# Performance work log

Hardware: AMD Instinct MI355X
Metric: run time of the kernel (lower is better)

The kernel has to match this reference:

```python
import jax, jax.numpy as jnp
import numpy as np


def setup_inputs() -> dict:
    key = jax.random.key(0)
    k1, k2, k3, k4 = jax.random.split(key, 4)
    B, C, H, W = 4, 512, 64, 64
    K = 20
    Cp = C // 4  # 128, proj_feat output channels
    feat = jax.random.normal(k1, (B, C, H, W), dtype=jnp.float32)
    cam = jax.random.uniform(k2, (B, K, H, W), dtype=jnp.float32)
    # 1x1 conv == linear over channel dim; store kernel as [Cout, Cin]
    w_proj = jax.random.normal(k3, (Cp, C), dtype=jnp.float32) * (1.0 / np.sqrt(C))
    b_proj = jax.random.normal(k4, (Cp,), dtype=jnp.float32) * 0.01
    return {"feat": feat, "cam": cam, "w_proj": w_proj, "b_proj": b_proj}


def reference(feat, cam, w_proj, b_proj):
    B, C, H, W = feat.shape
    K = cam.shape[1]
    N = H * W
    cam_detach = jax.lax.stop_gradient(cam)
    # proj_feat: 1x1 conv -> [B, N, C//4] token layout (matches view+transpose)
    feat_proj = jnp.einsum('bchw,oc->bhwo', feat, w_proj) + b_proj
    feat_proj = feat_proj.reshape(B, N, -1)                      # [B, N, Cp]
    cam_reshape = cam_detach.reshape(B, K, N)                    # [B, K, N]
    class_term = jnp.einsum('bkn,bnd->bkd', cam_reshape, feat_proj)  # [B, K, Cp]
    # unscaled self-attention over N pixels
    pixel_sim = jnp.einsum('bnd,bmd->bnm', feat_proj, feat_proj)     # [B, N, N]
    pixel_sim = jax.nn.softmax(pixel_sim, axis=-1)
    pixel_term = jnp.einsum('bnm,bmd->bnd', pixel_sim, feat_proj)    # [B, N, Cp]
    aug_cam = jnp.einsum('bkd,bnd->bkn', class_term, pixel_term)     # [B, K, N]
    return cam + aug_cam.reshape(B, K, H, W)
```

## Files before the change

### kernel.cpp

```cpp
#include <hip/hip_runtime.h>
#include <hip/hip_bf16.h>
#include <math.h>

#define NB 4
#define NC 512
#define NN 4096
#define NK 20
#define NCP 128
#define SPLIT 4
#define CHUNK (NN / SPLIT)
#define NTILES (CHUNK / 64)

typedef __bf16 bf16x8 __attribute__((ext_vector_type(8)));
typedef float f32x4 __attribute__((ext_vector_type(4)));
typedef float f32x16 __attribute__((ext_vector_type(16)));
typedef short short8 __attribute__((ext_vector_type(8)));
typedef unsigned int uint4v __attribute__((ext_vector_type(4)));

static __device__ __forceinline__ unsigned short f2bf(float f) {
    unsigned int u = __builtin_bit_cast(unsigned int, f);
    unsigned int r = (u + 0x7FFFu + ((u >> 16) & 1u)) >> 16;
    return (unsigned short)r;
}
static __device__ __forceinline__ float bf2f(unsigned short h) {
    unsigned int u = ((unsigned int)h) << 16;
    return __builtin_bit_cast(float, u);
}
static __device__ __forceinline__ bf16x8 ldbf8(const unsigned short* p) {
    return __builtin_bit_cast(bf16x8, *reinterpret_cast<const short8*>(p));
}
static __device__ __forceinline__ void gld16(const unsigned short* g, unsigned short* l) {
    __builtin_amdgcn_global_load_lds(
        (const __attribute__((address_space(1))) unsigned int*)g,
        (__attribute__((address_space(3))) unsigned int*)l, 16, 0, 0);
}
static __device__ __forceinline__ unsigned int cvtpk(float lo, float hi) {
    unsigned int r;
    asm("v_cvt_pk_bf16_f32 %0, %1, %2" : "=v"(r) : "v"(lo), "v"(hi));
    return r;
}

#define MFMA16(a, b, c) __builtin_amdgcn_mfma_f32_16x16x32_bf16(a, b, c, 0, 0, 0)
#define MFMA32(a, b, c) __builtin_amdgcn_mfma_f32_32x32x16_bf16(a, b, c, 0, 0, 0)
#define SCHED0() __builtin_amdgcn_sched_barrier(0)
#define BAR() do { SCHED0(); __builtin_amdgcn_s_barrier(); SCHED0(); } while (0)

__global__ __launch_bounds__(256) void proj_kernel(
    const float* __restrict__ feat, const float* __restrict__ w,
    const float* __restrict__ bias, unsigned short* __restrict__ fp,
    unsigned short* __restrict__ fpT)
{
    const int b = blockIdx.y;
    const int n0 = blockIdx.x * 64;
    const int tid = threadIdx.x;
    const int wid = tid >> 6;
    const int lane = tid & 63;
    const int lg = lane >> 4, lr = lane & 15;

    __shared__ unsigned short lds_f[2][64][40];

    const float* featb = feat + (size_t)b * NC * NN;

    f32x4 acc[2][4];
    #pragma unroll
    for (int i = 0; i < 2; ++i)
        #pragma unroll
        for (int j = 0; j < 4; ++j) acc[i][j] = (f32x4){0.f, 0.f, 0.f, 0.f};

    float4 pre[2];
    #pragma unroll
    for (int it = 0; it < 2; ++it) {
        int idx = it * 256 + tid;
        int cc = idx >> 4, q = idx & 15;
        pre[it] = *reinterpret_cast<const float4*>(&featb[(size_t)cc * NN + n0 + q * 4]);
    }

    for (int c0 = 0; c0 < NC; c0 += 32) {
        const int cur = (c0 >> 5) & 1;
        #pragma unroll
        for (int it = 0; it < 2; ++it) {
            int idx = it * 256 + tid;
            int cc = idx >> 4, q = idx & 15;
            float4 v = pre[it];
            lds_f[cur][q * 4 + 0][cc] = f2bf(v.x);
            lds_f[cur][q * 4 + 1][cc] = f2bf(v.y);
            lds_f[cur][q * 4 + 2][cc] = f2bf(v.z);
            lds_f[cur][q * 4 + 3][cc] = f2bf(v.w);
        }
        __syncthreads();
        if (c0 + 32 < NC) {
            #pragma unroll
            for (int it = 0; it < 2; ++it) {
                int idx = it * 256 + tid;
                int cc = idx >> 4, q = idx & 15;
                pre[it] = *reinterpret_cast<const float4*>(
                    &featb[(size_t)(c0 + 32 + cc) * NN + n0 + q * 4]);
            }
        }
        bf16x8 afr[2];
        #pragma unroll
        for (int dt = 0; dt < 2; ++dt) {
            const float4* wr = reinterpret_cast<const float4*>(
                w + (size_t)(wid * 32 + dt * 16 + lr) * NC + c0 + lg * 8);
            float4 w0 = wr[0], w1 = wr[1];
            short8 a;
            a[0] = (short)f2bf(w0.x); a[1] = (short)f2bf(w0.y);
            a[2] = (short)f2bf(w0.z); a[3] = (short)f2bf(w0.w);
            a[4] = (short)f2bf(w1.x); a[5] = (short)f2bf(w1.y);
            a[6] = (short)f2bf(w1.z); a[7] = (short)f2bf(w1.w);
            afr[dt] = __builtin_bit_cast(bf16x8, a);
        }
        #pragma unroll
        for (int n1 = 0; n1 < 4; ++n1) {
            bf16x8 bfr = ldbf8(&lds_f[cur][n1 * 16 + lr][lg * 8]);
            #pragma unroll
            for (int dt = 0; dt < 2; ++dt)
                acc[dt][n1] = MFMA16(afr[dt], bfr, acc[dt][n1]);
        }
    }
    #pragma unroll
    for (int dt = 0; dt < 2; ++dt)
        #pragma unroll
        for (int n1 = 0; n1 < 4; ++n1)
            #pragma unroll
            for (int i = 0; i < 4; ++i) {
                int d = wid * 32 + dt * 16 + lg * 4 + i;
                int n = n0 + n1 * 16 + lr;
                unsigned short h = f2bf(acc[dt][n1][i] + bias[d]);
                fp[((size_t)b * NN + n) * NCP + d] = h;
                fpT[((size_t)b * NCP + d) * NN + n] = h;
            }
}

__global__ __launch_bounds__(128) void ct_kernel(
    const float* __restrict__ cam, const unsigned short* __restrict__ fp,
    float* __restrict__ ct)
{
    const int bid = blockIdx.x;
    const int chunk = bid & 15;
    const int bk = bid >> 4;
    const int b = bk / NK, k = bk % NK;
    const int d2 = threadIdx.x & 63;
    const int half = threadIdx.x >> 6;
    const int nbase = chunk * 256 + half * 128;
    const float* camp = cam + ((size_t)b * NK + k) * NN + nbase;
    const unsigned short* fpp = fp + ((size_t)b * NN + nbase) * NCP + d2 * 2;
    float ax = 0.f, ay = 0.f;
    #pragma unroll 8
    for (int n = 0; n < 128; ++n) {
        float c = camp[n];
        unsigned int v = *reinterpret_cast<const unsigned int*>(&fpp[(size_t)n * NCP]);
        ax += c * bf2f((unsigned short)(v & 0xffff));
        ay += c * bf2f((unsigned short)(v >> 16));
    }
    float* ctp = &ct[((size_t)b * NK + k) * NCP + d2 * 2];
    atomicAdd(ctp, ax);
    atomicAdd(ctp + 1, ay);
}

__global__ __launch_bounds__(256, 2) void attn_partial_kernel(
    const unsigned short* __restrict__ fp, const unsigned short* __restrict__ fpT,
    unsigned short* __restrict__ po, float* __restrict__ mbuf, float* __restrict__ lbuf)
{
    const int b = blockIdx.z;
    const int sidx = blockIdx.y;
    const int tid = threadIdx.x;
    const int wid = tid >> 6;
    const int lane = tid & 63;
    const int l31 = lane & 31, hi = lane >> 5;
    const int q0 = blockIdx.x * 128 + wid * 32;
    const int kvbase = sidx * CHUNK;

    __shared__ unsigned short kt[2][64 * 128];
    __shared__ unsigned short vt[2][64 * 128];

    const unsigned short* fpb  = fp  + (size_t)b * NN * NCP;
    const unsigned short* fpTb = fpT + (size_t)b * NCP * NN;

    int offK[4], offV[4];
    #pragma unroll
    for (int i = 0; i < 4; ++i) {
        int oc = i * 256 + tid;
        int rk = oc >> 4, ck = oc & 15;
        offK[i] = rk * NCP + ((ck ^ (rk & 15)) << 3);
        int rowp = oc >> 4, cv = oc & 15;
        int cg = cv ^ (rowp & 15);
        int d = rowp * 2 + (cg >> 3), kvc = cg & 7;
        offV[i] = d * NN + (kvc << 3);
    }

    bf16x8 qf[8];
    #pragma unroll
    for (int kk = 0; kk < 8; ++kk)
        qf[kk] = ldbf8(&fpb[(size_t)(q0 + l31) * NCP + kk * 16 + hi * 8]);

    f32x16 o[4];
    #pragma unroll
    for (int dt = 0; dt < 4; ++dt)
        #pragma unroll
        for (int j = 0; j < 16; ++j) o[dt][j] = 0.f;
    float m_i = -INFINITY, l_i = 0.f;

    {
        const unsigned short* k0 = fpb + (size_t)kvbase * NCP;
        const unsigned short* v0 = fpTb + kvbase;
        #pragma unroll
        for (int i = 0; i < 4; ++i) {
            gld16(k0 + offK[i], &kt[0][(i * 256 + wid * 64) * 8]);
            gld16(v0 + offV[i], &vt[0][(i * 256 + wid * 64) * 8]);
        }
    }
    SCHED0();
    asm volatile("s_waitcnt vmcnt(0)" ::: "memory");
    BAR();

    for (int t = 0; t < NTILES; ++t) {
        const int cur = t & 1;
        {
            const int tn = (t + 1) & (NTILES - 1);
            const unsigned short* knext = fpb + (size_t)(kvbase + tn * 64) * NCP;
            const unsigned short* vnext = fpTb + kvbase + tn * 64;
            #pragma unroll
            for (int i = 0; i < 4; ++i) {
                gld16(knext + offK[i], &kt[cur ^ 1][(i * 256 + wid * 64) * 8]);
                gld16(vnext + offV[i], &vt[cur ^ 1][(i * 256 + wid * 64) * 8]);
            }
        }
        SCHED0();
        const unsigned short* ktc = &kt[cur][0];
        f32x16 s[2];
        #pragma unroll
        for (int g = 0; g < 2; ++g)
            #pragma unroll
            for (int j = 0; j < 16; ++j) s[g][j] = 0.f;
        __builtin_amdgcn_s_setprio(1);
        #pragma unroll
        for (int kk = 0; kk < 8; ++kk) {
            #pragma unroll
            for (int g = 0; g < 2; ++g) {
                int row = g * 32 + l31;
                bf16x8 kf = ldbf8(&ktc[row * 128 + (((kk * 2 + hi) ^ (row & 15)) << 3)]);
                s[g] = MFMA32(kf, qf[kk], s[g]);
            }
        }
        __builtin_amdgcn_s_setprio(0);
        float pmax = s[0][0];
        #pragma unroll
        for (int g = 0; g < 2; ++g)
            #pragma unroll
            for (int j = 0; j < 16; ++j) pmax = fmaxf(pmax, s[g][j]);
        pmax = fmaxf(pmax, __shfl_xor(pmax, 32));
        if (!__all(pmax - m_i <= 8.f)) {
            float mnew = fmaxf(m_i, pmax);
            float sc = __expf(m_i - mnew);
            l_i *= sc;
            #pragma unroll
            for (int dt = 0; dt < 4; ++dt)
                #pragma unroll
                for (int j = 0; j < 16; ++j) o[dt][j] *= sc;
            m_i = mnew;
        }
        float sum = 0.f;
        #pragma unroll
        for (int g = 0; g < 2; ++g)
            #pragma unroll
            for (int j = 0; j < 16; ++j) {
                float e = __expf(s[g][j] - m_i);
                s[g][j] = e;
                sum += e;
            }
        sum += __shfl_xor(sum, 32);
        l_i += sum;
        unsigned int wk[2][8];
        #pragma unroll
        for (int g = 0; g < 2; ++g)
            #pragma unroll
            for (int m = 0; m < 8; ++m)
                wk[g][m] = cvtpk(s[g][2 * m], s[g][2 * m + 1]);
        bf16x8 pf[4];
        #pragma unroll
        for (int g = 0; g < 2; ++g)
            #pragma unroll
            for (int sub = 0; sub < 2; ++sub) {
                unsigned int A0 = wk[g][4 * sub],     B0 = wk[g][4 * sub + 2];
                unsigned int A1 = wk[g][4 * sub + 1], B1 = wk[g][4 * sub + 3];
                asm("v_permlane32_swap_b32 %0, %1" : "+v"(A0), "+v"(B0));
                asm("v_permlane32_swap_b32 %0, %1" : "+v"(A1), "+v"(B1));
                uint4v u;
                u[0] = A0; u[1] = A1; u[2] = B0; u[3] = B1;
                pf[2 * g + sub] = __builtin_bit_cast(bf16x8, u);
            }
        const unsigned short* vtc = &vt[cur][0];
        __builtin_amdgcn_s_setprio(1);
        #pragma unroll
        for (int c2 = 0; c2 < 4; ++c2) {
            #pragma unroll
            for (int dt = 0; dt < 4; ++dt) {
                int row32 = dt * 32 + l31;
                int rowp = row32 >> 1;
                int chunk = (row32 & 1) * 8 + c2 * 2 + hi;
                bf16x8 vf = ldbf8(&vtc[rowp * 128 + ((chunk ^ (rowp & 15)) << 3)]);
                o[dt] = MFMA32(vf, pf[c2], o[dt]);
            }
        }
        __builtin_amdgcn_s_setprio(0);
        SCHED0();
        asm volatile("s_waitcnt vmcnt(0)" ::: "memory");
        BAR();
    }
    const size_t pbase = (size_t)(b * SPLIT + sidx) * NN + q0;
    const size_t rowoff = (pbase + l31) * NCP;
    #pragma unroll
    for (int dt = 0; dt < 4; ++dt)
        #pragma unroll
        for (int qd = 0; qd < 4; ++qd) {
            unsigned int u0 = cvtpk(o[dt][qd * 4 + 0], o[dt][qd * 4 + 1]);
            unsigned int u1 = cvtpk(o[dt][qd * 4 + 2], o[dt][qd * 4 + 3]);
            *reinterpret_cast<uint2*>(&po[rowoff + dt * 32 + qd * 8 + hi * 4]) =
                make_uint2(u0, u1);
        }
    if (hi == 0) {
        mbuf[pbase + l31] = m_i;
        lbuf[pbase + l31] = l_i;
    }
}

__global__ __launch_bounds__(256) void aug_kernel(
    const float* __restrict__ cam, const float* __restrict__ ct,
    const unsigned short* __restrict__ po, const float* __restrict__ mbuf,
    const float* __restrict__ lbuf, float* __restrict__ out)
{
    const int b = blockIdx.y;
    const int tid = threadIdx.x, wid = tid >> 6, lane = tid & 63;
    const int lg = lane >> 4, lr = lane & 15;
    const int n0 = blockIdx.x * 64 + wid * 16;
    const int row = n0 + lr;
    const float* ctb = ct + (size_t)b * NK * NCP;

    float m_s[SPLIT], l_s[SPLIT], M = -INFINITY;
    #pragma unroll
    for (int s = 0; s < SPLIT; ++s) {
        m_s[s] = mbuf[(size_t)(b * SPLIT + s) * NN + row];
        l_s[s] = lbuf[(size_t)(b * SPLIT + s) * NN + row];
        M = fmaxf(M, m_s[s]);
    }
    float L = 0.f, wgt[SPLIT];
    #pragma unroll
    for (int s = 0; s < SPLIT; ++s) { wgt[s] = __expf(m_s[s] - M); L += wgt[s] * l_s[s]; }
    const float inv = 1.f / L;
    #pragma unroll
    for (int s = 0; s < SPLIT; ++s) wgt[s] *= inv;

    f32x4 acc[2];
    acc[0] = (f32x4){0.f, 0.f, 0.f, 0.f};
    acc[1] = (f32x4){0.f, 0.f, 0.f, 0.f};
    #pragma unroll
    for (int kk = 0; kk < 4; ++kk) {
        float mg[8];
        #pragma unroll
        for (int j = 0; j < 8; ++j) mg[j] = 0.f;
        #pragma unroll
        for (int s = 0; s < SPLIT; ++s) {
            uint4v v = *reinterpret_cast<const uint4v*>(
                &po[((size_t)(b * SPLIT + s) * NN + row) * NCP + kk * 32 + lg * 8]);
            #pragma unroll
            for (int j = 0; j < 4; ++j) {
                mg[2 * j]     += wgt[s] * bf2f((unsigned short)(v[j] & 0xffff));
                mg[2 * j + 1] += wgt[s] * bf2f((unsigned short)(v[j] >> 16));
            }
        }
        uint4v au;
        #pragma unroll
        for (int j = 0; j < 4; ++j) au[j] = cvtpk(mg[2 * j], mg[2 * j + 1]);
        bf16x8 af = __builtin_bit_cast(bf16x8, au);
        #pragma unroll
        for (int c = 0; c < 2; ++c) {
            int k = c * 16 + lr;
            short8 bv;
            if (k < NK) {
                const float* cr = &ctb[(size_t)k * NCP + kk * 32 + lg * 8];
                #pragma unroll
                for (int j = 0; j < 8; ++j) bv[j] = (short)f2bf(cr[j]);
            } else {
                #pragma unroll
                for (int j = 0; j < 8; ++j) bv[j] = 0;
            }
            acc[c] = MFMA16(af, __builtin_bit_cast(bf16x8, bv), acc[c]);
        }
    }
    #pragma unroll
    for (int c = 0; c < 2; ++c) {
        int k = c * 16 + lr;
        if (k < NK) {
            #pragma unroll
            for (int i = 0; i < 4; ++i) {
                size_t off = ((size_t)b * NK + k) * NN + n0 + lg * 4 + i;
                out[off] = cam[off] + acc[c][i];
            }
        }
    }
}

extern "C" void kernel_launch(void* const* d_in, const int* in_sizes, int n_in,
                              void* d_out, int out_size, void* d_ws, size_t ws_size,
                              hipStream_t stream) {
    const float* feat = (const float*)d_in[0];
    const float* cam  = (const float*)d_in[1];
    const float* wpr  = (const float*)d_in[2];
    const float* bpr  = (const float*)d_in[3];
    float* out = (float*)d_out;

    const size_t MB = 1024 * 1024;
    char* ws = (char*)d_ws;
    unsigned short* fp  = (unsigned short*)(ws);
    unsigned short* fpT = (unsigned short*)(ws + 4 * MB);
    float* ct           = (float*)(ws + 12 * MB);
    unsigned short* po  = (unsigned short*)(ws + 13 * MB);
    float* mbuf         = (float*)(ws + 30 * MB);
    float* lbuf         = (float*)(ws + 31 * MB);

    hipMemsetAsync(ct, 0, (size_t)NB * NK * NCP * sizeof(float), stream);
    proj_kernel<<<dim3(NN / 64, NB), 256, 0, stream>>>(feat, wpr, bpr, fp, fpT);
    ct_kernel<<<NB * NK * 16, 128, 0, stream>>>(cam, fp, ct);
    attn_partial_kernel<<<dim3(NN / 128, SPLIT, NB), 256, 0, stream>>>(fp, fpT, po, mbuf, lbuf);
    aug_kernel<<<dim3(NN / 64, NB), 256, 0, stream>>>(cam, ct, po, mbuf, lbuf, out);
}
```

Measured before the change: 94.96 us.

## Fuse class-term reduction into attention kernel using shared K tiles

Result: faster. 90.23 us (-5.0%).

```diff
diff --git a/kernel.cpp b/kernel.cpp
--- a/kernel.cpp
+++ b/kernel.cpp
@@ -132,34 +132,9 @@
             }
 }
 
-__global__ __launch_bounds__(128) void ct_kernel(
-    const float* __restrict__ cam, const unsigned short* __restrict__ fp,
-    float* __restrict__ ct)
-{
-    const int bid = blockIdx.x;
-    const int chunk = bid & 15;
-    const int bk = bid >> 4;
-    const int b = bk / NK, k = bk % NK;
-    const int d2 = threadIdx.x & 63;
-    const int half = threadIdx.x >> 6;
-    const int nbase = chunk * 256 + half * 128;
-    const float* camp = cam + ((size_t)b * NK + k) * NN + nbase;
-    const unsigned short* fpp = fp + ((size_t)b * NN + nbase) * NCP + d2 * 2;
-    float ax = 0.f, ay = 0.f;
-    #pragma unroll 8
-    for (int n = 0; n < 128; ++n) {
-        float c = camp[n];
-        unsigned int v = *reinterpret_cast<const unsigned int*>(&fpp[(size_t)n * NCP]);
-        ax += c * bf2f((unsigned short)(v & 0xffff));
-        ay += c * bf2f((unsigned short)(v >> 16));
-    }
-    float* ctp = &ct[((size_t)b * NK + k) * NCP + d2 * 2];
-    atomicAdd(ctp, ax);
-    atomicAdd(ctp + 1, ay);
-}
-
 __global__ __launch_bounds__(256, 2) void attn_partial_kernel(
     const unsigned short* __restrict__ fp, const unsigned short* __restrict__ fpT,
+    const float* __restrict__ cam, float* __restrict__ ctg,
     unsigned short* __restrict__ po, float* __restrict__ mbuf, float* __restrict__ lbuf)
 {
     const int b = blockIdx.z;
@@ -177,6 +152,12 @@
     const unsigned short* fpb  = fp  + (size_t)b * NN * NCP;
     const unsigned short* fpTb = fpT + (size_t)b * NCP * NN;
 
+    const bool doCT = (blockIdx.x < NK);
+    const int pd = tid & 63;
+    const int qtr = tid >> 6;
+    const float* camb = cam + ((size_t)b * NK + blockIdx.x) * NN + kvbase;
+    float ctx = 0.f, cty = 0.f;
+
     int offK[4], offV[4];
     #pragma unroll
     for (int i = 0; i < 4; ++i) {
@@ -244,6 +225,19 @@
             }
         }
         __builtin_amdgcn_s_setprio(0);
+        if (doCT) {
+            const float* camt = camb + t * 64 + qtr * 16;
+            const int c8 = pd >> 2, de = (pd * 2) & 7;
+            #pragma unroll
+            for (int n = 0; n < 16; ++n) {
+                int rown = qtr * 16 + n;
+                float cv = camt[n];
+                unsigned int v = *reinterpret_cast<const unsigned int*>(
+                    &ktc[rown * 128 + ((c8 ^ (rown & 15)) << 3) + de]);
+                ctx += cv * bf2f((unsigned short)(v & 0xffff));
+                cty += cv * bf2f((unsigned short)(v >> 16));
+            }
+        }
         float pmax = s[0][0];
         #pragma unroll
         for (int g = 0; g < 2; ++g)
@@ -322,6 +316,11 @@
     if (hi == 0) {
         mbuf[pbase + l31] = m_i;
         lbuf[pbase + l31] = l_i;
+    }
+    if (doCT) {
+        float* ctp = &ctg[((size_t)b * NK + blockIdx.x) * NCP + pd * 2];
+        atomicAdd(ctp, ctx);
+        atomicAdd(ctp + 1, cty);
     }
 }
 
@@ -421,7 +420,7 @@
 
     hipMemsetAsync(ct, 0, (size_t)NB * NK * NCP * sizeof(float), stream);
     proj_kernel<<<dim3(NN / 64, NB), 256, 0, stream>>>(feat, wpr, bpr, fp, fpT);
-    ct_kernel<<<NB * NK * 16, 128, 0, stream>>>(cam, fp, ct);
-    attn_partial_kernel<<<dim3(NN / 128, SPLIT, NB), 256, 0, stream>>>(fp, fpT, po, mbuf, lbuf);
+    attn_partial_kernel<<<dim3(NN / 128, SPLIT, NB), 256, 0, stream>>>(
+        fp, fpT, cam, ct, po, mbuf, lbuf);
     aug_kernel<<<dim3(NN / 64, NB), 256, 0, stream>>>(cam, ct, po, mbuf, lbuf, out);
 }
```
